# Performance work log

Measured on AMD Instinct MI355X. Metric: run time of the kernel, lower is better.

The kernel has to match this reference:

```python
import jax, jax.numpy as jnp
import numpy as np

N_NODES = 100000
N_EDGES = 600000
H = 128


def setup_inputs() -> dict:
    key = jax.random.key(0)
    k_z, k_e, k_w1, k_w2 = jax.random.split(key, 4)
    z = jax.random.normal(k_z, (N_NODES, H), dtype=jnp.float32)
    edge_index = jax.random.randint(k_e, (2, N_EDGES), 0, N_NODES, dtype=jnp.int64)
    # Kaiming-ish init scale for the MLP weights
    W1 = jax.random.normal(k_w1, (2 * H, H), dtype=jnp.float32) * (1.0 / np.sqrt(2 * H))
    b1 = jnp.zeros((H,), dtype=jnp.float32)
    W2 = jax.random.normal(k_w2, (H, 1), dtype=jnp.float32) * (1.0 / np.sqrt(H))
    b2 = jnp.zeros((1,), dtype=jnp.float32)
    return {"z": z, "edge_index": edge_index, "W1": W1, "b1": b1, "W2": W2, "b2": b2}


def reference(z, edge_index, W1, b1, W2, b2):
    # Gather source/destination node embeddings: [E, H] each
    src = z[edge_index[0]]
    dst = z[edge_index[1]]
    # Avoid materializing the [E, 2H] concat: split W1 into src/dst blocks
    # so fc1(cat(src,dst)) == src @ W1[:H] + dst @ W1[H:] + b1
    h = src @ W1[:H] + dst @ W1[H:] + b1  # [E, H]
    h = jax.nn.relu(h)
    out = h @ W2 + b2  # [E, 1]
    return out.reshape(-1)
```

## Files before the change

kernel.cpp:

```cpp
#include <hip/hip_runtime.h>
#include <hip/hip_bf16.h>
#include <stdint.h>

#define N_NODES_C 100000
#define N_EDGES_C 600000
#define H_C 128

typedef __bf16 bf16x8 __attribute__((ext_vector_type(8)));
typedef float f32x16 __attribute__((ext_vector_type(16)));
typedef float f32x4v __attribute__((ext_vector_type(4)));
typedef _Float16 half8 __attribute__((ext_vector_type(8)));
typedef unsigned short ushort8 __attribute__((ext_vector_type(8)));

__device__ __forceinline__ unsigned short f2bf(float f) {
    unsigned int u = __builtin_bit_cast(unsigned int, f);
    u += 0x7fffu + ((u >> 16) & 1u);
    return (unsigned short)(u >> 16);
}

__launch_bounds__(256, 2)
__global__ void node_gemm_kernel(const float* __restrict__ z,
                                 const float* __restrict__ W1,
                                 const float* __restrict__ b1,
                                 _Float16* __restrict__ uv) {
    const int lane = threadIdx.x & 63;
    const int wv   = threadIdx.x >> 6;
    const int l31  = lane & 31;
    const int half = lane >> 5;
    const int uh   = wv >> 1;

    bf16x8 bfrag[8][2];
    float  badd[2];
    int    ncol[2];
    #pragma unroll
    for (int t = 0; t < 2; ++t) {
        int n2  = (wv * 2 + t) * 32 + l31;
        ncol[t] = n2 - uh * 128;
        badd[t] = uh ? 0.0f : b1[n2];
        const float* wcol = W1 + (size_t)(uh ? 128 : 0) * H_C + ncol[t];
        #pragma unroll
        for (int s = 0; s < 8; ++s) {
            ushort8 au;
            #pragma unroll
            for (int j = 0; j < 8; ++j) {
                int k = s * 16 + half * 8 + j;
                au[j] = f2bf(wcol[(size_t)k * H_C]);
            }
            bfrag[s][t] = __builtin_bit_cast(bf16x8, au);
        }
    }
    const size_t segbase = uh ? (size_t)N_NODES_C * H_C : 0;

    for (int tile = blockIdx.x; tile < N_NODES_C / 32; tile += gridDim.x) {
        const float* arow = z + (size_t)(tile * 32 + l31) * H_C + half * 8;

        f32x4v alo[8], ahi[8];
        #pragma unroll
        for (int s = 0; s < 8; ++s) {
            alo[s] = *reinterpret_cast<const f32x4v*>(arow + s * 16);
            ahi[s] = *reinterpret_cast<const f32x4v*>(arow + s * 16 + 4);
        }

        f32x16 acc[2] = {};
        #pragma unroll
        for (int s = 0; s < 8; ++s) {
            ushort8 au;
            #pragma unroll
            for (int j = 0; j < 4; ++j) {
                au[j]     = f2bf(alo[s][j]);
                au[j + 4] = f2bf(ahi[s][j]);
            }
            bf16x8 a = __builtin_bit_cast(bf16x8, au);
            acc[0] = __builtin_amdgcn_mfma_f32_32x32x16_bf16(a, bfrag[s][0], acc[0], 0, 0, 0);
            acc[1] = __builtin_amdgcn_mfma_f32_32x32x16_bf16(a, bfrag[s][1], acc[1], 0, 0, 0);
        }

        const int node0 = tile * 32;
        #pragma unroll
        for (int t = 0; t < 2; ++t) {
            #pragma unroll
            for (int r = 0; r < 16; ++r) {
                int row = (r & 3) + 8 * (r >> 2) + 4 * half;
                float v = acc[t][r] + badd[t];
                float fo = __shfl_xor(v, 1);
                if ((lane & 1) == 0) {
                    unsigned int pk = __builtin_bit_cast(
                        unsigned int, __builtin_amdgcn_cvt_pkrtz(v, fo));
                    size_t idx = segbase + (size_t)(node0 + row) * H_C + ncol[t];
                    *reinterpret_cast<unsigned int*>(uv + idx) = pk;
                }
            }
        }
    }
}

__global__ void edge_kernel(const _Float16* __restrict__ uv,
                            const int* __restrict__ ei,
                            const float* __restrict__ w2,
                            const float* __restrict__ b2,
                            float* __restrict__ out) {
    const int tid = blockIdx.x * blockDim.x + threadIdx.x;
    const int j   = tid & 15;
    const int q   = tid >> 4;
    const int e0  = q * 8;
    if (e0 >= N_EDGES_C) return;

    float w2v[8];
    {
        f32x4v a = *reinterpret_cast<const f32x4v*>(w2 + j * 8);
        f32x4v b = *reinterpret_cast<const f32x4v*>(w2 + j * 8 + 4);
        #pragma unroll
        for (int k = 0; k < 4; ++k) { w2v[k] = a[k]; w2v[k + 4] = b[k]; }
    }
    const float c2 = b2[0];
    const _Float16* vbase = uv + (size_t)N_NODES_C * H_C;

    int4 sa = *reinterpret_cast<const int4*>(ei + e0);
    int4 sb = *reinterpret_cast<const int4*>(ei + e0 + 4);
    int4 da = *reinterpret_cast<const int4*>(ei + N_EDGES_C + e0);
    int4 db = *reinterpret_cast<const int4*>(ei + N_EDGES_C + e0 + 4);

    int se[8] = { sa.x, sa.y, sa.z, sa.w, sb.x, sb.y, sb.z, sb.w };
    int de[8] = { da.x, da.y, da.z, da.w, db.x, db.y, db.z, db.w };

    half8 uu[8], vv[8];
    #pragma unroll
    for (int i = 0; i < 8; ++i) {
        uu[i] = *reinterpret_cast<const half8*>(uv    + (size_t)se[i] * H_C + j * 8);
        vv[i] = *reinterpret_cast<const half8*>(vbase + (size_t)de[i] * H_C + j * 8);
    }

    float p[8];
    #pragma unroll
    for (int i = 0; i < 8; ++i) {
        float acc = 0.0f;
        #pragma unroll
        for (int k = 0; k < 8; ++k) {
            float h = (float)uu[i][k] + (float)vv[i][k];
            h = h > 0.0f ? h : 0.0f;
            acc = fmaf(h, w2v[k], acc);
        }
        p[i] = acc;
    }
    #pragma unroll
    for (int m = 1; m <= 8; m <<= 1) {
        #pragma unroll
        for (int i = 0; i < 8; ++i) p[i] += __shfl_xor(p[i], m);
    }
    if (j == 0) {
        float4 o0 = { p[0] + c2, p[1] + c2, p[2] + c2, p[3] + c2 };
        float4 o1 = { p[4] + c2, p[5] + c2, p[6] + c2, p[7] + c2 };
        *reinterpret_cast<float4*>(out + e0)     = o0;
        *reinterpret_cast<float4*>(out + e0 + 4) = o1;
    }
}

extern "C" void kernel_launch(void* const* d_in, const int* in_sizes, int n_in,
                              void* d_out, int out_size, void* d_ws, size_t ws_size,
                              hipStream_t stream) {
    const float* z  = (const float*)d_in[0];
    const int*   ei = (const int*)d_in[1];
    const float* W1 = (const float*)d_in[2];
    const float* b1 = (const float*)d_in[3];
    const float* W2 = (const float*)d_in[4];
    const float* b2 = (const float*)d_in[5];
    float* out = (float*)d_out;

    _Float16* uv = (_Float16*)d_ws;

    node_gemm_kernel<<<1024, 256, 0, stream>>>(z, W1, b1, uv);

    int nquarters = N_EDGES_C / 8;
    edge_kernel<<<(nquarters * 16 + 255) / 256, 256, 0, stream>>>(uv, ei, W2, b2, out);
}
```

Baseline: 171.0 us.

## Prepack W1 into MFMA fragment layout and stage z tiles through LDS

```diff
diff --git a/kernel.cpp b/kernel.cpp
--- a/kernel.cpp
+++ b/kernel.cpp
@@ -12,83 +12,107 @@
 typedef _Float16 half8 __attribute__((ext_vector_type(8)));
 typedef unsigned short ushort8 __attribute__((ext_vector_type(8)));
 
+#define LDS_STRIDE 136
+
 __device__ __forceinline__ unsigned short f2bf(float f) {
     unsigned int u = __builtin_bit_cast(unsigned int, f);
     u += 0x7fffu + ((u >> 16) & 1u);
     return (unsigned short)(u >> 16);
 }
 
+__global__ void w1fmt_kernel(const float* __restrict__ W1,
+                             unsigned short* __restrict__ w1f) {
+    int i = blockIdx.x * blockDim.x + threadIdx.x;
+    if (i >= 8 * 8 * 64 * 8) return;
+    int j = i & 7;
+    int L = (i >> 3) & 63;
+    int t = (i >> 9) & 7;
+    int s = (i >> 12) & 7;
+    int k  = s * 16 + ((L >> 5) * 8) + j;
+    int n2 = t * 32 + (L & 31);
+    float w = (n2 < 128) ? W1[k * H_C + n2]
+                         : W1[(128 + k) * H_C + (n2 - 128)];
+    w1f[i] = f2bf(w);
+}
+
 __launch_bounds__(256, 2)
 __global__ void node_gemm_kernel(const float* __restrict__ z,
-                                 const float* __restrict__ W1,
+                                 const unsigned short* __restrict__ w1f,
                                  const float* __restrict__ b1,
                                  _Float16* __restrict__ uv) {
+    __shared__ unsigned short smem[32 * LDS_STRIDE];
+
     const int lane = threadIdx.x & 63;
     const int wv   = threadIdx.x >> 6;
     const int l31  = lane & 31;
     const int half = lane >> 5;
     const int uh   = wv >> 1;
+    const int tile = blockIdx.x;
+
+    {
+        const int sr = threadIdx.x >> 3;
+        const int sc = (threadIdx.x & 7) * 16;
+        const float* src = z + (size_t)(tile * 32 + sr) * H_C + sc;
+        f32x4v f0 = *reinterpret_cast<const f32x4v*>(src);
+        f32x4v f1 = *reinterpret_cast<const f32x4v*>(src + 4);
+        f32x4v f2 = *reinterpret_cast<const f32x4v*>(src + 8);
+        f32x4v f3 = *reinterpret_cast<const f32x4v*>(src + 12);
+        ushort8 lo, hi;
+        #pragma unroll
+        for (int j = 0; j < 4; ++j) {
+            lo[j]     = f2bf(f0[j]);
+            lo[j + 4] = f2bf(f1[j]);
+            hi[j]     = f2bf(f2[j]);
+            hi[j + 4] = f2bf(f3[j]);
+        }
+        *reinterpret_cast<ushort8*>(smem + sr * LDS_STRIDE + sc)     = lo;
+        *reinterpret_cast<ushort8*>(smem + sr * LDS_STRIDE + sc + 8) = hi;
+    }
 
     bf16x8 bfrag[8][2];
-    float  badd[2];
-    int    ncol[2];
+    #pragma unroll
+    for (int s = 0; s < 8; ++s) {
+        #pragma unroll
+        for (int t = 0; t < 2; ++t) {
+            bfrag[s][t] = reinterpret_cast<const bf16x8*>(w1f)
+                              [(s * 8 + wv * 2 + t) * 64 + lane];
+        }
+    }
+
+    float badd[2];
+    int   ncol[2];
     #pragma unroll
     for (int t = 0; t < 2; ++t) {
         int n2  = (wv * 2 + t) * 32 + l31;
         ncol[t] = n2 - uh * 128;
         badd[t] = uh ? 0.0f : b1[n2];
-        const float* wcol = W1 + (size_t)(uh ? 128 : 0) * H_C + ncol[t];
-        #pragma unroll
-        for (int s = 0; s < 8; ++s) {
-            ushort8 au;
-            #pragma unroll
-            for (int j = 0; j < 8; ++j) {
-                int k = s * 16 + half * 8 + j;
-                au[j] = f2bf(wcol[(size_t)k * H_C]);
-            }
-            bfrag[s][t] = __builtin_bit_cast(bf16x8, au);
-        }
     }
     const size_t segbase = uh ? (size_t)N_NODES_C * H_C : 0;
 
-    for (int tile = blockIdx.x; tile < N_NODES_C / 32; tile += gridDim.x) {
-        const float* arow = z + (size_t)(tile * 32 + l31) * H_C + half * 8;
-
-        f32x4v alo[8], ahi[8];
-        #pragma unroll
-        for (int s = 0; s < 8; ++s) {
-            alo[s] = *reinterpret_cast<const f32x4v*>(arow + s * 16);
-            ahi[s] = *reinterpret_cast<const f32x4v*>(arow + s * 16 + 4);
-        }
-
-        f32x16 acc[2] = {};
-        #pragma unroll
-        for (int s = 0; s < 8; ++s) {
-            ushort8 au;
-            #pragma unroll
-            for (int j = 0; j < 4; ++j) {
-                au[j]     = f2bf(alo[s][j]);
-                au[j + 4] = f2bf(ahi[s][j]);
-            }
-            bf16x8 a = __builtin_bit_cast(bf16x8, au);
-            acc[0] = __builtin_amdgcn_mfma_f32_32x32x16_bf16(a, bfrag[s][0], acc[0], 0, 0, 0);
-            acc[1] = __builtin_amdgcn_mfma_f32_32x32x16_bf16(a, bfrag[s][1], acc[1], 0, 0, 0);
-        }
-
-        const int node0 = tile * 32;
-        #pragma unroll
-        for (int t = 0; t < 2; ++t) {
-            #pragma unroll
-            for (int r = 0; r < 16; ++r) {
-                int row = (r & 3) + 8 * (r >> 2) + 4 * half;
-                float v = acc[t][r] + badd[t];
-                float fo = __shfl_xor(v, 1);
-                if ((lane & 1) == 0) {
-                    unsigned int pk = __builtin_bit_cast(
-                        unsigned int, __builtin_amdgcn_cvt_pkrtz(v, fo));
-                    size_t idx = segbase + (size_t)(node0 + row) * H_C + ncol[t];
-                    *reinterpret_cast<unsigned int*>(uv + idx) = pk;
-                }
+    __syncthreads();
+
+    f32x16 acc[2] = {};
+    #pragma unroll
+    for (int s = 0; s < 8; ++s) {
+        bf16x8 a = *reinterpret_cast<const bf16x8*>(
+                       smem + l31 * LDS_STRIDE + s * 16 + half * 8);
+        acc[0] = __builtin_amdgcn_mfma_f32_32x32x16_bf16(a, bfrag[s][0], acc[0], 0, 0, 0);
+        acc[1] = __builtin_amdgcn_mfma_f32_32x32x16_bf16(a, bfrag[s][1], acc[1], 0, 0, 0);
+    }
+
+    const int node0 = tile * 32;
+    #pragma unroll
+    for (int t = 0; t < 2; ++t) {
+        #pragma unroll
+        for (int r = 0; r < 16; ++r) {
+            int row = (r & 3) + 8 * (r >> 2) + 4 * half;
+            float v = acc[t][r] + badd[t];
+            float fo = __shfl_xor(v, 1);
+            if ((lane & 1) == 0) {
+                unsigned int pk = __builtin_bit_cast(
+                    unsigned int, __builtin_amdgcn_cvt_pkrtz(v, fo));
+                size_t idx = segbase + (size_t)(node0 + row) * H_C + ncol[t];
+                *reinterpret_cast<unsigned int*>(uv + idx) = pk;
             }
         }
     }
@@ -166,9 +190,12 @@
     const float* b2 = (const float*)d_in[5];
     float* out = (float*)d_out;
 
-    _Float16* uv = (_Float16*)d_ws;
-
-    node_gemm_kernel<<<1024, 256, 0, stream>>>(z, W1, b1, uv);
+    unsigned short* w1f = (unsigned short*)d_ws;
+    _Float16* uv = (_Float16*)((char*)d_ws + 65536);
+
+    w1fmt_kernel<<<(8 * 8 * 64 * 8 + 255) / 256, 256, 0, stream>>>(W1, w1f);
+
+    node_gemm_kernel<<<N_NODES_C / 32, 256, 0, stream>>>(z, w1f, b1, uv);
 
     int nquarters = N_EDGES_C / 8;
     edge_kernel<<<(nquarters * 16 + 255) / 256, 256, 0, stream>>>(uv, ei, W2, b2, out);
```

New measurement: 151.0 us (median of 2 runs). 1.13x faster.
